# Kernel optimization log

Measured on AMD Instinct MI355X. Metric: run time of the kernel, lower is better.

Reference implementation:

```python
import jax, jax.numpy as jnp
import numpy as np

DIM = 2048        # model hidden size
INTER = 1408      # per-expert intermediate size
E = 16            # n_routed_experts
TOPK = 2          # n_activated_experts
S_INTER = 2816    # shared experts intermediate (n_shared_experts * INTER)
T = 4096          # tokens (batch*seq, module flattens to [-1, dim])
ROUTE_SCALE = 1.0


def setup_inputs() -> dict:
    key = jax.random.key(0)
    ks = jax.random.split(key, 8)
    g = lambda k, shape, scale: (jax.random.normal(k, shape, dtype=jnp.float32) * scale)
    return {
        "x": g(ks[0], (T, DIM), 1.0),
        "gate_w": g(ks[1], (E, DIM), 0.02),
        "w1": g(ks[2], (E, INTER, DIM), 0.02),
        "w2": g(ks[3], (E, DIM, INTER), 0.02),
        "w3": g(ks[4], (E, INTER, DIM), 0.02),
        "sw1": g(ks[5], (S_INTER, DIM), 0.02),
        "sw2": g(ks[6], (DIM, S_INTER), 0.02),
        "sw3": g(ks[7], (S_INTER, DIM), 0.02),
    }


def _moe_forward(x, gate_w, w1, w2, w3, sw1, sw2, sw3):
    t = x.shape[0]
    # ---- gate: softmax scores -> top-k experts per token ----
    scores = jax.nn.softmax(x @ gate_w.T, axis=-1)          # [T, E]
    top_w, top_i = jax.lax.top_k(scores, TOPK)              # [T, K]
    top_w = top_w * ROUTE_SCALE
    # dense combine weights [T, E]: zero for unselected experts
    combine = jnp.zeros((t, E), x.dtype).at[jnp.arange(t)[:, None], top_i].add(top_w)
    # ---- routed experts: gated silu MLP per expert, weighted combine ----
    # loop over the small fixed expert count; tokens with combine==0 contribute 0,
    # matching the original scatter/gather dispatch math exactly.
    y = jnp.zeros_like(x)
    for e in range(E):
        h = jax.nn.silu(x @ w1[e].T) * (x @ w3[e].T)        # [T, INTER]
        y = y + (h @ w2[e].T) * combine[:, e:e + 1]
    # ---- shared experts ----
    z = (jax.nn.silu(x @ sw1.T) * (x @ sw3.T)) @ sw2.T      # [T, DIM]
    return y + z


def reference(x, gate_w, w1, w2, w3, sw1, sw2, sw3):
    return _moe_forward(x, gate_w, w1, w2, w3, sw1, sw2, sw3)
```

## Files before the change

kernel.cpp:

```cpp
#include <hip/hip_runtime.h>
#include <hip/hip_bf16.h>
#include <cstdint>
#include <cstddef>

#define TTOK   4096
#define DIM_   2048
#define INTER_ 1408
#define NEXP   16
#define SINTER_ 2816
#define BM 128
#define BN 128
#define BK 32
#define MAXROWS (TTOK*2 + NEXP*BM)
#define MAXMT   (TTOK*2/BM + NEXP)

typedef unsigned short u16;
typedef __attribute__((ext_vector_type(8))) short short8;
typedef __attribute__((ext_vector_type(4))) float f32x4;

#define AS3P(p) ((__attribute__((address_space(3))) void*)(p))
#define AS1P(p) ((const __attribute__((address_space(1))) void*)(p))

__device__ __forceinline__ void gll16(const void* g, void* l) {
    __builtin_amdgcn_global_load_lds(AS1P(g), AS3P(l), 16, 0, 0);
}

__device__ __forceinline__ u16 f2bf(float f) {
    __hip_bfloat16 h = __float2bfloat16(f);
    union { __hip_bfloat16 h; u16 u; } c; c.h = h; return c.u;
}

__device__ __forceinline__ unsigned pk2(float a, float b) {
    unsigned r;
    asm("v_cvt_pk_bf16_f32 %0, %1, %2" : "=v"(r) : "v"(a), "v"(b));
    return r;
}

__device__ __forceinline__ short8 cvt8(float4 q0, float4 q1) {
    union { int4 i; short8 s; } u;
    u.i = make_int4((int)pk2(q0.x, q0.y), (int)pk2(q0.z, q0.w),
                    (int)pk2(q1.x, q1.y), (int)pk2(q1.z, q1.w));
    return u.s;
}

__device__ __forceinline__ int4 pack8(float4 a, float4 b) {
    int4 r;
    r.x = (int)pk2(a.x, a.y);
    r.y = (int)pk2(a.z, a.w);
    r.z = (int)pk2(b.x, b.y);
    r.w = (int)pk2(b.z, b.w);
    return r;
}


__global__ void init_kernel(int* perm_rt, float* pw_rt, int* perm_sh, int* misc, int* zrow) {
    int i = blockIdx.x * 256 + threadIdx.x;
    if (i < MAXROWS) { perm_rt[i] = -1; pw_rt[i] = 0.f; }
    if (i < TTOK)    perm_sh[i] = i;
    if (i < 32)      misc[i] = 0;
    if (i < 1024)    zrow[i] = 0;
}

__global__ void cvt_kernel(const float* __restrict__ s, u16* __restrict__ d, int n8) {
    int stride = gridDim.x * 256;
    for (int i = blockIdx.x * 256 + threadIdx.x; i < n8; i += stride) {
        const float4* s4 = (const float4*)(s + (size_t)i * 8);
        float4 a = s4[0], b = s4[1];
        *(int4*)(d + (size_t)i * 8) = pack8(a, b);
    }
}

__global__ void gate_kernel(const float* __restrict__ x, const float* __restrict__ gw,
                            int* __restrict__ topi, float* __restrict__ topw,
                            int* __restrict__ misc) {
    int t = blockIdx.x;
    int lane = threadIdx.x;
    const float* xr = x + (size_t)t * DIM_;
    float acc[NEXP];
#pragma unroll
    for (int e = 0; e < NEXP; e++) acc[e] = 0.f;
#pragma unroll
    for (int i = 0; i < 8; i++) {
        int k = i * 256 + lane * 4;
        float4 xv = *(const float4*)(xr + k);
#pragma unroll
        for (int e = 0; e < NEXP; e++) {
            float4 gv = *(const float4*)(gw + (size_t)e * DIM_ + k);
            acc[e] += xv.x * gv.x + xv.y * gv.y + xv.z * gv.z + xv.w * gv.w;
        }
    }
#pragma unroll
    for (int e = 0; e < NEXP; e++) {
        float v = acc[e];
        for (int off = 32; off > 0; off >>= 1) v += __shfl_down(v, off);
        acc[e] = v;
    }
    if (lane == 0) {
        float m = acc[0];
#pragma unroll
        for (int e = 1; e < NEXP; e++) m = fmaxf(m, acc[e]);
        float p[NEXP]; float s = 0.f;
#pragma unroll
        for (int e = 0; e < NEXP; e++) { p[e] = __expf(acc[e] - m); s += p[e]; }
        int i0 = 0; float v0 = p[0];
#pragma unroll
        for (int e = 1; e < NEXP; e++) if (p[e] > v0) { v0 = p[e]; i0 = e; }
        int i1 = -1; float v1 = -1.f;
#pragma unroll
        for (int e = 0; e < NEXP; e++) if (e != i0 && p[e] > v1) { v1 = p[e]; i1 = e; }
        float inv = 1.f / s;
        topi[2 * t] = i0; topi[2 * t + 1] = i1;
        topw[2 * t] = v0 * inv; topw[2 * t + 1] = v1 * inv;
        atomicAdd(&misc[i0], 1);
        atomicAdd(&misc[i1], 1);
    }
}

__global__ void scan_kernel(int* misc) {
    int* counts = misc;
    int* base   = misc + 32;
    int* te     = misc + 48;
    int* tr     = misc + 128;
    int b = 0, tt = 0;
    for (int e = 0; e < NEXP; e++) {
        int c = counts[e];
        int nt = (c + BM - 1) >> 7;
        base[e] = b;
        for (int i = 0; i < nt; i++) { te[tt] = e; tr[tt] = b + i * BM; tt++; }
        b += nt * BM;
    }
    for (int i = tt; i < MAXMT; i++) te[i] = -1;
}

__global__ void scatter_kernel(const int* __restrict__ topi, const float* __restrict__ topw,
                               int* __restrict__ misc, int* __restrict__ perm,
                               float* __restrict__ pw) {
    int t = blockIdx.x * 256 + threadIdx.x;
    if (t >= TTOK) return;
    int* fill = misc + 16;
    int* base = misc + 32;
#pragma unroll
    for (int k = 0; k < 2; k++) {
        int e = topi[2 * t + k];
        int pos = base[e] + atomicAdd(&fill[e], 1);
        perm[pos] = t;
        pw[pos] = topw[2 * t + k];
    }
}


template<bool GROUPED>
__global__ __launch_bounds__(256, 2) void gemm_h13_k(
    const u16* __restrict__ Xb,
    const float* __restrict__ W1b, const float* __restrict__ W3b,
    u16* __restrict__ H,
    const int* __restrict__ perm,
    const int* __restrict__ te, const int* __restrict__ tr,
    const u16* __restrict__ zrow,
    int N, int K, int nt_m, int chunk)
{
    const int q = (blockIdx.x & 7) * chunk + (blockIdx.x >> 3);
    if (q >= nt_m * (N / BN)) return;
    const int jn = q / nt_m, im = q % nt_m;
    int e, slot0;
    if (GROUPED) { e = te[im]; if (e < 0) return; slot0 = tr[im]; }
    else         { e = 0; slot0 = im * BM; }
    const int n0 = jn * BN;
    const float* W1 = W1b + (size_t)e * N * K;
    const float* W3 = W3b + (size_t)e * N * K;

    __shared__ __align__(16) u16   As[BM * BK];
    __shared__ __align__(16) float B1f[BM * BK];
    __shared__ __align__(16) float B3f[BM * BK];

    const int tid = threadIdx.x;
    const int lane = tid & 63, wid = tid >> 6;
    const int wr = wid >> 1, wc = wid & 1;
    const int col = lane & 15, kg = lane >> 4;

    const int aRow = wid * 32 + (lane >> 2);
    const int aCk  = ((lane & 3) ^ ((lane >> 3) & 3)) * 8;
    const int ta0 = perm[slot0 + aRow];
    const int ta1 = perm[slot0 + aRow + 16];
    const u16* ga0 = (ta0 >= 0 ? Xb + (size_t)ta0 * K : zrow) + aCk;
    const u16* ga1 = (ta1 >= 0 ? Xb + (size_t)ta1 * K : zrow) + aCk;
    u16* la0 = As + (wid * 32) * BK;
    u16* la1 = As + (wid * 32 + 16) * BK;

    const int bRowL = lane >> 3;
    const int bCk   = ((lane & 7) ^ bRowL) * 4;
    const float* g1 = W1 + (size_t)(n0 + wid * 32 + bRowL) * K + bCk;
    const float* g3 = W3 + (size_t)(n0 + wid * 32 + bRowL) * K + bCk;
    float* lb1 = B1f + (wid * 32) * BK;
    float* lb3 = B3f + (wid * 32) * BK;

    const int aswz = (col >> 1) & 3;
    const int bswz = col & 7;

    f32x4 acc1[4][4] = {};
    f32x4 acc3[4][4] = {};

    for (int k0 = 0; k0 < K; k0 += BK) {
        gll16(ga0 + k0, la0);
        gll16(ga1 + k0, la1);
#pragma unroll
        for (int j = 0; j < 4; j++) {
            gll16(g1 + (size_t)j * 8 * K + k0, lb1 + j * 8 * BK);
            gll16(g3 + (size_t)j * 8 * K + k0, lb3 + j * 8 * BK);
        }
        __syncthreads();

        short8 a[4];
#pragma unroll
        for (int mi = 0; mi < 4; mi++)
            a[mi] = *(const short8*)(As + (wr * 64 + mi * 16 + col) * BK + ((kg ^ aswz) * 8));
#pragma unroll
        for (int ni = 0; ni < 4; ni++) {
            const int rowB = wc * 64 + ni * 16 + col;
            const float* rb1 = B1f + rowB * BK;
            const float* rb3 = B3f + rowB * BK;
            const int c0 = ((kg * 2) ^ bswz) * 4;
            const int c1 = ((kg * 2 + 1) ^ bswz) * 4;
            short8 v1 = cvt8(*(const float4*)(rb1 + c0), *(const float4*)(rb1 + c1));
            short8 v3 = cvt8(*(const float4*)(rb3 + c0), *(const float4*)(rb3 + c1));
#pragma unroll
            for (int mi = 0; mi < 4; mi++) {
                acc1[mi][ni] = __builtin_amdgcn_mfma_f32_16x16x32_bf16(a[mi], v1, acc1[mi][ni], 0, 0, 0);
                acc3[mi][ni] = __builtin_amdgcn_mfma_f32_16x16x32_bf16(a[mi], v3, acc3[mi][ni], 0, 0, 0);
            }
        }
        __syncthreads();
    }

#pragma unroll
    for (int mi = 0; mi < 4; mi++) {
#pragma unroll
        for (int j = 0; j < 4; j++) {
            int row = slot0 + wr * 64 + mi * 16 + kg * 4 + j;
#pragma unroll
            for (int ni = 0; ni < 4; ni++) {
                float v1 = acc1[mi][ni][j];
                float v3 = acc3[mi][ni][j];
                float hv = v1 / (1.f + __expf(-v1)) * v3;
                int c = n0 + wc * 64 + ni * 16 + col;
                H[(size_t)row * N + c] = f2bf(hv);
            }
        }
    }
}

template<bool ATOMIC>
__global__ __launch_bounds__(256, 2) void gemm_out_k(
    const u16* __restrict__ Hm,
    const float* __restrict__ W2b,
    float* __restrict__ Out,
    const int* __restrict__ perm, const float* __restrict__ pw,
    const int* __restrict__ te, const int* __restrict__ tr,
    int K, int nt_m, int chunk)
{
    const int q = (blockIdx.x & 7) * chunk + (blockIdx.x >> 3);
    if (q >= nt_m * (DIM_ / BN)) return;
    const int jn = q / nt_m, im = q % nt_m;
    int e, slot0;
    if (ATOMIC) { e = te[im]; if (e < 0) return; slot0 = tr[im]; }
    else        { e = 0; slot0 = im * BM; }
    const int n0 = jn * BN;
    const float* W2 = W2b + (size_t)e * DIM_ * K;

    __shared__ __align__(16) u16   As[BM * BK];
    __shared__ __align__(16) float Bf[BM * BK];

    const int tid = threadIdx.x;
    const int lane = tid & 63, wid = tid >> 6;
    const int wr = wid >> 1, wc = wid & 1;
    const int col = lane & 15, kg = lane >> 4;

    const int aRow = wid * 32 + (lane >> 2);
    const int aCk  = ((lane & 3) ^ ((lane >> 3) & 3)) * 8;
    const u16* ga0 = Hm + (size_t)(slot0 + aRow) * K + aCk;
    const u16* ga1 = Hm + (size_t)(slot0 + aRow + 16) * K + aCk;
    u16* la0 = As + (wid * 32) * BK;
    u16* la1 = As + (wid * 32 + 16) * BK;

    const int bRowL = lane >> 3;
    const int bCk   = ((lane & 7) ^ bRowL) * 4;
    const float* g2 = W2 + (size_t)(n0 + wid * 32 + bRowL) * K + bCk;
    float* lb = Bf + (wid * 32) * BK;

    const int aswz = (col >> 1) & 3;
    const int bswz = col & 7;

    f32x4 acc[4][4] = {};

    for (int k0 = 0; k0 < K; k0 += BK) {
        gll16(ga0 + k0, la0);
        gll16(ga1 + k0, la1);
#pragma unroll
        for (int j = 0; j < 4; j++)
            gll16(g2 + (size_t)j * 8 * K + k0, lb + j * 8 * BK);
        __syncthreads();

        short8 a[4];
#pragma unroll
        for (int mi = 0; mi < 4; mi++)
            a[mi] = *(const short8*)(As + (wr * 64 + mi * 16 + col) * BK + ((kg ^ aswz) * 8));
#pragma unroll
        for (int ni = 0; ni < 4; ni++) {
            const int rowB = wc * 64 + ni * 16 + col;
            const float* rb = Bf + rowB * BK;
            const int c0 = ((kg * 2) ^ bswz) * 4;
            const int c1 = ((kg * 2 + 1) ^ bswz) * 4;
            short8 bv = cvt8(*(const float4*)(rb + c0), *(const float4*)(rb + c1));
#pragma unroll
            for (int mi = 0; mi < 4; mi++)
                acc[mi][ni] = __builtin_amdgcn_mfma_f32_16x16x32_bf16(a[mi], bv, acc[mi][ni], 0, 0, 0);
        }
        __syncthreads();
    }

#pragma unroll
    for (int mi = 0; mi < 4; mi++) {
#pragma unroll
        for (int j = 0; j < 4; j++) {
            int rloc = wr * 64 + mi * 16 + kg * 4 + j;
            int slot = slot0 + rloc;
            if (ATOMIC) {
                int token = perm[slot];
                if (token < 0) continue;
                float w = pw[slot];
#pragma unroll
                for (int ni = 0; ni < 4; ni++) {
                    int c = n0 + wc * 64 + ni * 16 + col;
                    atomicAdd(&Out[(size_t)token * DIM_ + c], acc[mi][ni][j] * w);
                }
            } else {
#pragma unroll
                for (int ni = 0; ni < 4; ni++) {
                    int c = n0 + wc * 64 + ni * 16 + col;
                    Out[(size_t)slot * DIM_ + c] = acc[mi][ni][j];
                }
            }
        }
    }
}


extern "C" void kernel_launch(void* const* d_in, const int* in_sizes, int n_in,
                              void* d_out, int out_size, void* d_ws, size_t ws_size,
                              hipStream_t stream) {
    (void)in_sizes; (void)n_in; (void)out_size; (void)ws_size;
    const float* x   = (const float*)d_in[0];
    const float* gw  = (const float*)d_in[1];
    const float* w1  = (const float*)d_in[2];
    const float* w2  = (const float*)d_in[3];
    const float* w3  = (const float*)d_in[4];
    const float* sw1 = (const float*)d_in[5];
    const float* sw2 = (const float*)d_in[6];
    const float* sw3 = (const float*)d_in[7];
    float* out = (float*)d_out;

    char* ws = (char*)d_ws;
    size_t off = 0;
    auto take = [&](size_t bytes) -> void* {
        void* p = ws + off;
        off += (bytes + 255) & ~(size_t)255;
        return p;
    };
    u16*   xb      = (u16*)take((size_t)TTOK * DIM_ * 2);
    u16*   hbuf    = (u16*)take((size_t)MAXROWS * INTER_ * 2);
    int*   perm_rt = (int*)take((size_t)MAXROWS * 4);
    float* pw_rt   = (float*)take((size_t)MAXROWS * 4);
    int*   perm_sh = (int*)take((size_t)TTOK * 4);
    int*   topi    = (int*)take((size_t)TTOK * 2 * 4);
    float* topw    = (float*)take((size_t)TTOK * 2 * 4);
    int*   misc    = (int*)take(1024);
    int*   zrow    = (int*)take(4096);

    init_kernel<<<MAXROWS / 256, 256, 0, stream>>>(perm_rt, pw_rt, perm_sh, misc, zrow);
    cvt_kernel<<<512, 256, 0, stream>>>(x, xb, TTOK * DIM_ / 8);
    gate_kernel<<<TTOK, 64, 0, stream>>>(x, gw, topi, topw, misc);
    scan_kernel<<<1, 1, 0, stream>>>(misc);
    scatter_kernel<<<TTOK / 256, 256, 0, stream>>>(topi, topw, misc, perm_rt, pw_rt);

    auto grid8 = [](int total) { return ((total + 7) / 8) * 8; };
    auto chunk8 = [](int total) { return (total + 7) / 8; };

    {
        int total = (TTOK / BM) * (SINTER_ / BN);
        gemm_h13_k<false><<<grid8(total), 256, 0, stream>>>(
            xb, sw1, sw3, hbuf, perm_sh, nullptr, nullptr, (const u16*)zrow,
            SINTER_, DIM_, TTOK / BM, chunk8(total));
    }
    {
        int total = (TTOK / BM) * (DIM_ / BN);
        gemm_out_k<false><<<grid8(total), 256, 0, stream>>>(
            hbuf, sw2, out, nullptr, nullptr, nullptr, nullptr,
            SINTER_, TTOK / BM, chunk8(total));
    }
    {
        int total = MAXMT * (INTER_ / BN);
        gemm_h13_k<true><<<grid8(total), 256, 0, stream>>>(
            xb, w1, w3, hbuf, perm_rt, misc + 48, misc + 128, (const u16*)zrow,
            INTER_, DIM_, MAXMT, chunk8(total));
    }
    {
        int total = MAXMT * (DIM_ / BN);
        gemm_out_k<true><<<grid8(total), 256, 0, stream>>>(
            hbuf, w2, out, perm_rt, pw_rt, misc + 48, misc + 128,
            INTER_, MAXMT, chunk8(total));
    }
}
```

Before: 879.0 us.

## Double-buffer LDS tiles in gate/up and down GEMMs to overlap loads with MFMA

Both GEMM kernels now keep two LDS buffers per operand. The next K-tile is issued via global_load_lds before computing on the current tile, and an explicit vmcnt(0) wait plus barrier replaces the two syncthreads per iteration. The aim is to hide global memory latency behind the MFMA work. The cost is double the LDS footprint: the gate/up kernel goes from about 40KB to 80KB, which may reduce occupancy.

Result: no change. 876.5 us (-0.3%).

```diff
diff --git a/kernel.cpp b/kernel.cpp
--- a/kernel.cpp
+++ b/kernel.cpp
@@ -51,6 +51,12 @@
     r.w = (int)pk2(b.z, b.w);
     return r;
 }
+
+#define WAIT_VM0_BARRIER() do { \
+    asm volatile("s_waitcnt vmcnt(0)" ::: "memory"); \
+    __builtin_amdgcn_s_barrier(); \
+    asm volatile("" ::: "memory"); \
+} while (0)
 
 
 __global__ void init_kernel(int* perm_rt, float* pw_rt, int* perm_sh, int* misc, int* zrow) {
@@ -169,9 +175,9 @@
     const float* W1 = W1b + (size_t)e * N * K;
     const float* W3 = W3b + (size_t)e * N * K;
 
-    __shared__ __align__(16) u16   As[BM * BK];
-    __shared__ __align__(16) float B1f[BM * BK];
-    __shared__ __align__(16) float B3f[BM * BK];
+    __shared__ __align__(16) u16   As[2][BM * BK];
+    __shared__ __align__(16) float B1f[2][BM * BK];
+    __shared__ __align__(16) float B3f[2][BM * BK];
 
     const int tid = threadIdx.x;
     const int lane = tid & 63, wid = tid >> 6;
@@ -184,15 +190,14 @@
     const int ta1 = perm[slot0 + aRow + 16];
     const u16* ga0 = (ta0 >= 0 ? Xb + (size_t)ta0 * K : zrow) + aCk;
     const u16* ga1 = (ta1 >= 0 ? Xb + (size_t)ta1 * K : zrow) + aCk;
-    u16* la0 = As + (wid * 32) * BK;
-    u16* la1 = As + (wid * 32 + 16) * BK;
+    const int laOff0 = (wid * 32) * BK;
+    const int laOff1 = (wid * 32 + 16) * BK;
 
     const int bRowL = lane >> 3;
     const int bCk   = ((lane & 7) ^ bRowL) * 4;
     const float* g1 = W1 + (size_t)(n0 + wid * 32 + bRowL) * K + bCk;
     const float* g3 = W3 + (size_t)(n0 + wid * 32 + bRowL) * K + bCk;
-    float* lb1 = B1f + (wid * 32) * BK;
-    float* lb3 = B3f + (wid * 32) * BK;
+    const int lbOff = (wid * 32) * BK;
 
     const int aswz = (col >> 1) & 3;
     const int bswz = col & 7;
@@ -200,25 +205,44 @@
     f32x4 acc1[4][4] = {};
     f32x4 acc3[4][4] = {};
 
+    {
+        gll16(ga0, &As[0][laOff0]);
+        gll16(ga1, &As[0][laOff1]);
+#pragma unroll
+        for (int j = 0; j < 4; j++) {
+            gll16(g1 + (size_t)j * 8 * K, &B1f[0][lbOff + j * 8 * BK]);
+            gll16(g3 + (size_t)j * 8 * K, &B3f[0][lbOff + j * 8 * BK]);
+        }
+    }
+    WAIT_VM0_BARRIER();
+
+    int cur = 0;
     for (int k0 = 0; k0 < K; k0 += BK) {
-        gll16(ga0 + k0, la0);
-        gll16(ga1 + k0, la1);
-#pragma unroll
-        for (int j = 0; j < 4; j++) {
-            gll16(g1 + (size_t)j * 8 * K + k0, lb1 + j * 8 * BK);
-            gll16(g3 + (size_t)j * 8 * K + k0, lb3 + j * 8 * BK);
-        }
-        __syncthreads();
+        const int kn = k0 + BK;
+        if (kn < K) {
+            const int nb = cur ^ 1;
+            gll16(ga0 + kn, &As[nb][laOff0]);
+            gll16(ga1 + kn, &As[nb][laOff1]);
+#pragma unroll
+            for (int j = 0; j < 4; j++) {
+                gll16(g1 + (size_t)j * 8 * K + kn, &B1f[nb][lbOff + j * 8 * BK]);
+                gll16(g3 + (size_t)j * 8 * K + kn, &B3f[nb][lbOff + j * 8 * BK]);
+            }
+        }
+
+        const u16*   Ac  = As[cur];
+        const float* B1c = B1f[cur];
+        const float* B3c = B3f[cur];
 
         short8 a[4];
 #pragma unroll
         for (int mi = 0; mi < 4; mi++)
-            a[mi] = *(const short8*)(As + (wr * 64 + mi * 16 + col) * BK + ((kg ^ aswz) * 8));
+            a[mi] = *(const short8*)(Ac + (wr * 64 + mi * 16 + col) * BK + ((kg ^ aswz) * 8));
 #pragma unroll
         for (int ni = 0; ni < 4; ni++) {
             const int rowB = wc * 64 + ni * 16 + col;
-            const float* rb1 = B1f + rowB * BK;
-            const float* rb3 = B3f + rowB * BK;
+            const float* rb1 = B1c + rowB * BK;
+            const float* rb3 = B3c + rowB * BK;
             const int c0 = ((kg * 2) ^ bswz) * 4;
             const int c1 = ((kg * 2 + 1) ^ bswz) * 4;
             short8 v1 = cvt8(*(const float4*)(rb1 + c0), *(const float4*)(rb1 + c1));
@@ -229,7 +253,9 @@
                 acc3[mi][ni] = __builtin_amdgcn_mfma_f32_16x16x32_bf16(a[mi], v3, acc3[mi][ni], 0, 0, 0);
             }
         }
-        __syncthreads();
+
+        WAIT_VM0_BARRIER();
+        cur ^= 1;
     }
 
 #pragma unroll
@@ -267,8 +293,8 @@
     const int n0 = jn * BN;
     const float* W2 = W2b + (size_t)e * DIM_ * K;
 
-    __shared__ __align__(16) u16   As[BM * BK];
-    __shared__ __align__(16) float Bf[BM * BK];
+    __shared__ __align__(16) u16   As[2][BM * BK];
+    __shared__ __align__(16) float Bf[2][BM * BK];
 
     const int tid = threadIdx.x;
     const int lane = tid & 63, wid = tid >> 6;
@@ -279,35 +305,51 @@
     const int aCk  = ((lane & 3) ^ ((lane >> 3) & 3)) * 8;
     const u16* ga0 = Hm + (size_t)(slot0 + aRow) * K + aCk;
     const u16* ga1 = Hm + (size_t)(slot0 + aRow + 16) * K + aCk;
-    u16* la0 = As + (wid * 32) * BK;
-    u16* la1 = As + (wid * 32 + 16) * BK;
+    const int laOff0 = (wid * 32) * BK;
+    const int laOff1 = (wid * 32 + 16) * BK;
 
     const int bRowL = lane >> 3;
     const int bCk   = ((lane & 7) ^ bRowL) * 4;
     const float* g2 = W2 + (size_t)(n0 + wid * 32 + bRowL) * K + bCk;
-    float* lb = Bf + (wid * 32) * BK;
+    const int lbOff = (wid * 32) * BK;
 
     const int aswz = (col >> 1) & 3;
     const int bswz = col & 7;
 
     f32x4 acc[4][4] = {};
 
+    {
+        gll16(ga0, &As[0][laOff0]);
+        gll16(ga1, &As[0][laOff1]);
+#pragma unroll
+        for (int j = 0; j < 4; j++)
+            gll16(g2 + (size_t)j * 8 * K, &Bf[0][lbOff + j * 8 * BK]);
+    }
+    WAIT_VM0_BARRIER();
+
+    int cur = 0;
     for (int k0 = 0; k0 < K; k0 += BK) {
-        gll16(ga0 + k0, la0);
-        gll16(ga1 + k0, la1);
-#pragma unroll
-        for (int j = 0; j < 4; j++)
-            gll16(g2 + (size_t)j * 8 * K + k0, lb + j * 8 * BK);
-        __syncthreads();
+        const int kn = k0 + BK;
+        if (kn < K) {
+            const int nb = cur ^ 1;
+            gll16(ga0 + kn, &As[nb][laOff0]);
+            gll16(ga1 + kn, &As[nb][laOff1]);
+#pragma unroll
+            for (int j = 0; j < 4; j++)
+                gll16(g2 + (size_t)j * 8 * K + kn, &Bf[nb][lbOff + j * 8 * BK]);
+        }
+
+        const u16*   Ac = As[cur];
+        const float* Bc = Bf[cur];
 
         short8 a[4];
 #pragma unroll
         for (int mi = 0; mi < 4; mi++)
-            a[mi] = *(const short8*)(As + (wr * 64 + mi * 16 + col) * BK + ((kg ^ aswz) * 8));
+            a[mi] = *(const short8*)(Ac + (wr * 64 + mi * 16 + col) * BK + ((kg ^ aswz) * 8));
 #pragma unroll
         for (int ni = 0; ni < 4; ni++) {
             const int rowB = wc * 64 + ni * 16 + col;
-            const float* rb = Bf + rowB * BK;
+            const float* rb = Bc + rowB * BK;
             const int c0 = ((kg * 2) ^ bswz) * 4;
             const int c1 = ((kg * 2 + 1) ^ bswz) * 4;
             short8 bv = cvt8(*(const float4*)(rb + c0), *(const float4*)(rb + c1));
@@ -315,7 +357,9 @@
             for (int mi = 0; mi < 4; mi++)
                 acc[mi][ni] = __builtin_amdgcn_mfma_f32_16x16x32_bf16(a[mi], bv, acc[mi][ni], 0, 0, 0);
         }
-        __syncthreads();
+
+        WAIT_VM0_BARRIER();
+        cur ^= 1;
     }
 
 #pragma unroll
```

## Pre-convert all weight matrices to bf16 before the GEMMs

Applied to the files above, without the earlier changes.

Adds per-call conversion passes that turn the fp32 expert and shared weights into bf16 workspace buffers. The GEMM kernels now load bf16 B tiles straight into LDS with the same swizzle as the A tiles, so the per-tile fp32-to-bf16 conversion in the inner loop goes away and weight bytes per tile load are halved. The cost is a full extra read and write over roughly 600MB of fp32 weights on every call, plus a larger workspace. The cvt launch grid for x is also enlarged.

After: 864.0 us. About the same (-1.7%).

```diff
diff --git a/kernel.cpp b/kernel.cpp
--- a/kernel.cpp
+++ b/kernel.cpp
@@ -34,13 +34,6 @@
     unsigned r;
     asm("v_cvt_pk_bf16_f32 %0, %1, %2" : "=v"(r) : "v"(a), "v"(b));
     return r;
-}
-
-__device__ __forceinline__ short8 cvt8(float4 q0, float4 q1) {
-    union { int4 i; short8 s; } u;
-    u.i = make_int4((int)pk2(q0.x, q0.y), (int)pk2(q0.z, q0.w),
-                    (int)pk2(q1.x, q1.y), (int)pk2(q1.z, q1.w));
-    return u.s;
 }
 
 __device__ __forceinline__ int4 pack8(float4 a, float4 b) {
@@ -152,7 +145,7 @@
 template<bool GROUPED>
 __global__ __launch_bounds__(256, 2) void gemm_h13_k(
     const u16* __restrict__ Xb,
-    const float* __restrict__ W1b, const float* __restrict__ W3b,
+    const u16* __restrict__ W1b, const u16* __restrict__ W3b,
     u16* __restrict__ H,
     const int* __restrict__ perm,
     const int* __restrict__ te, const int* __restrict__ tr,
@@ -166,36 +159,37 @@
     if (GROUPED) { e = te[im]; if (e < 0) return; slot0 = tr[im]; }
     else         { e = 0; slot0 = im * BM; }
     const int n0 = jn * BN;
-    const float* W1 = W1b + (size_t)e * N * K;
-    const float* W3 = W3b + (size_t)e * N * K;
-
-    __shared__ __align__(16) u16   As[BM * BK];
-    __shared__ __align__(16) float B1f[BM * BK];
-    __shared__ __align__(16) float B3f[BM * BK];
+    const u16* W1 = W1b + (size_t)e * N * K;
+    const u16* W3 = W3b + (size_t)e * N * K;
+
+    __shared__ __align__(16) u16 As[BM * BK];
+    __shared__ __align__(16) u16 B1s[BM * BK];
+    __shared__ __align__(16) u16 B3s[BM * BK];
 
     const int tid = threadIdx.x;
     const int lane = tid & 63, wid = tid >> 6;
     const int wr = wid >> 1, wc = wid & 1;
     const int col = lane & 15, kg = lane >> 4;
 
-    const int aRow = wid * 32 + (lane >> 2);
-    const int aCk  = ((lane & 3) ^ ((lane >> 3) & 3)) * 8;
-    const int ta0 = perm[slot0 + aRow];
-    const int ta1 = perm[slot0 + aRow + 16];
-    const u16* ga0 = (ta0 >= 0 ? Xb + (size_t)ta0 * K : zrow) + aCk;
-    const u16* ga1 = (ta1 >= 0 ? Xb + (size_t)ta1 * K : zrow) + aCk;
-    u16* la0 = As + (wid * 32) * BK;
-    u16* la1 = As + (wid * 32 + 16) * BK;
-
-    const int bRowL = lane >> 3;
-    const int bCk   = ((lane & 7) ^ bRowL) * 4;
-    const float* g1 = W1 + (size_t)(n0 + wid * 32 + bRowL) * K + bCk;
-    const float* g3 = W3 + (size_t)(n0 + wid * 32 + bRowL) * K + bCk;
-    float* lb1 = B1f + (wid * 32) * BK;
-    float* lb3 = B3f + (wid * 32) * BK;
-
-    const int aswz = (col >> 1) & 3;
-    const int bswz = col & 7;
+    const int lr = lane >> 2;
+    const int kb = ((lane & 3) ^ ((lane >> 3) & 3)) * 8;
+    const int ar0 = wid * 32 + lr, ar1 = ar0 + 16;
+    const int ta0 = perm[slot0 + ar0];
+    const int ta1 = perm[slot0 + ar1];
+    const u16* ga0 = (ta0 >= 0 ? Xb + (size_t)ta0 * K : zrow) + kb;
+    const u16* ga1 = (ta1 >= 0 ? Xb + (size_t)ta1 * K : zrow) + kb;
+    const u16* gb1a = W1 + (size_t)(n0 + ar0) * K + kb;
+    const u16* gb1b = W1 + (size_t)(n0 + ar1) * K + kb;
+    const u16* gb3a = W3 + (size_t)(n0 + ar0) * K + kb;
+    const u16* gb3b = W3 + (size_t)(n0 + ar1) * K + kb;
+    u16* la0 = As  + (wid * 32) * BK;
+    u16* la1 = As  + (wid * 32 + 16) * BK;
+    u16* lb1a = B1s + (wid * 32) * BK;
+    u16* lb1b = B1s + (wid * 32 + 16) * BK;
+    u16* lb3a = B3s + (wid * 32) * BK;
+    u16* lb3b = B3s + (wid * 32 + 16) * BK;
+
+    const int sw = (col >> 1) & 3;
 
     f32x4 acc1[4][4] = {};
     f32x4 acc3[4][4] = {};
@@ -203,26 +197,21 @@
     for (int k0 = 0; k0 < K; k0 += BK) {
         gll16(ga0 + k0, la0);
         gll16(ga1 + k0, la1);
-#pragma unroll
-        for (int j = 0; j < 4; j++) {
-            gll16(g1 + (size_t)j * 8 * K + k0, lb1 + j * 8 * BK);
-            gll16(g3 + (size_t)j * 8 * K + k0, lb3 + j * 8 * BK);
-        }
+        gll16(gb1a + k0, lb1a);
+        gll16(gb1b + k0, lb1b);
+        gll16(gb3a + k0, lb3a);
+        gll16(gb3b + k0, lb3b);
         __syncthreads();
 
         short8 a[4];
 #pragma unroll
         for (int mi = 0; mi < 4; mi++)
-            a[mi] = *(const short8*)(As + (wr * 64 + mi * 16 + col) * BK + ((kg ^ aswz) * 8));
+            a[mi] = *(const short8*)(As + (wr * 64 + mi * 16 + col) * BK + ((kg ^ sw) * 8));
 #pragma unroll
         for (int ni = 0; ni < 4; ni++) {
-            const int rowB = wc * 64 + ni * 16 + col;
-            const float* rb1 = B1f + rowB * BK;
-            const float* rb3 = B3f + rowB * BK;
-            const int c0 = ((kg * 2) ^ bswz) * 4;
-            const int c1 = ((kg * 2 + 1) ^ bswz) * 4;
-            short8 v1 = cvt8(*(const float4*)(rb1 + c0), *(const float4*)(rb1 + c1));
-            short8 v3 = cvt8(*(const float4*)(rb3 + c0), *(const float4*)(rb3 + c1));
+            const int rowB = (wc * 64 + ni * 16 + col) * BK + ((kg ^ sw) * 8);
+            short8 v1 = *(const short8*)(B1s + rowB);
+            short8 v3 = *(const short8*)(B3s + rowB);
 #pragma unroll
             for (int mi = 0; mi < 4; mi++) {
                 acc1[mi][ni] = __builtin_amdgcn_mfma_f32_16x16x32_bf16(a[mi], v1, acc1[mi][ni], 0, 0, 0);
@@ -252,7 +241,7 @@
 template<bool ATOMIC>
 __global__ __launch_bounds__(256, 2) void gemm_out_k(
     const u16* __restrict__ Hm,
-    const float* __restrict__ W2b,
+    const u16* __restrict__ W2b,
     float* __restrict__ Out,
     const int* __restrict__ perm, const float* __restrict__ pw,
     const int* __restrict__ te, const int* __restrict__ tr,
@@ -265,52 +254,46 @@
     if (ATOMIC) { e = te[im]; if (e < 0) return; slot0 = tr[im]; }
     else        { e = 0; slot0 = im * BM; }
     const int n0 = jn * BN;
-    const float* W2 = W2b + (size_t)e * DIM_ * K;
-
-    __shared__ __align__(16) u16   As[BM * BK];
-    __shared__ __align__(16) float Bf[BM * BK];
+    const u16* W2 = W2b + (size_t)e * DIM_ * K;
+
+    __shared__ __align__(16) u16 As[BM * BK];
+    __shared__ __align__(16) u16 Bs[BM * BK];
 
     const int tid = threadIdx.x;
     const int lane = tid & 63, wid = tid >> 6;
     const int wr = wid >> 1, wc = wid & 1;
     const int col = lane & 15, kg = lane >> 4;
 
-    const int aRow = wid * 32 + (lane >> 2);
-    const int aCk  = ((lane & 3) ^ ((lane >> 3) & 3)) * 8;
-    const u16* ga0 = Hm + (size_t)(slot0 + aRow) * K + aCk;
-    const u16* ga1 = Hm + (size_t)(slot0 + aRow + 16) * K + aCk;
+    const int lr = lane >> 2;
+    const int kb = ((lane & 3) ^ ((lane >> 3) & 3)) * 8;
+    const int ar0 = wid * 32 + lr, ar1 = ar0 + 16;
+    const u16* ga0 = Hm + (size_t)(slot0 + ar0) * K + kb;
+    const u16* ga1 = Hm + (size_t)(slot0 + ar1) * K + kb;
+    const u16* gb0 = W2 + (size_t)(n0 + ar0) * K + kb;
+    const u16* gb1 = W2 + (size_t)(n0 + ar1) * K + kb;
     u16* la0 = As + (wid * 32) * BK;
     u16* la1 = As + (wid * 32 + 16) * BK;
-
-    const int bRowL = lane >> 3;
-    const int bCk   = ((lane & 7) ^ bRowL) * 4;
-    const float* g2 = W2 + (size_t)(n0 + wid * 32 + bRowL) * K + bCk;
-    float* lb = Bf + (wid * 32) * BK;
-
-    const int aswz = (col >> 1) & 3;
-    const int bswz = col & 7;
+    u16* lb0 = Bs + (wid * 32) * BK;
+    u16* lb1 = Bs + (wid * 32 + 16) * BK;
+
+    const int sw = (col >> 1) & 3;
 
     f32x4 acc[4][4] = {};
 
     for (int k0 = 0; k0 < K; k0 += BK) {
         gll16(ga0 + k0, la0);
         gll16(ga1 + k0, la1);
-#pragma unroll
-        for (int j = 0; j < 4; j++)
-            gll16(g2 + (size_t)j * 8 * K + k0, lb + j * 8 * BK);
+        gll16(gb0 + k0, lb0);
+        gll16(gb1 + k0, lb1);
         __syncthreads();
 
         short8 a[4];
 #pragma unroll
         for (int mi = 0; mi < 4; mi++)
-            a[mi] = *(const short8*)(As + (wr * 64 + mi * 16 + col) * BK + ((kg ^ aswz) * 8));
+            a[mi] = *(const short8*)(As + (wr * 64 + mi * 16 + col) * BK + ((kg ^ sw) * 8));
 #pragma unroll
         for (int ni = 0; ni < 4; ni++) {
-            const int rowB = wc * 64 + ni * 16 + col;
-            const float* rb = Bf + rowB * BK;
-            const int c0 = ((kg * 2) ^ bswz) * 4;
-            const int c1 = ((kg * 2 + 1) ^ bswz) * 4;
-            short8 bv = cvt8(*(const float4*)(rb + c0), *(const float4*)(rb + c1));
+            short8 bv = *(const short8*)(Bs + (wc * 64 + ni * 16 + col) * BK + ((kg ^ sw) * 8));
 #pragma unroll
             for (int mi = 0; mi < 4; mi++)
                 acc[mi][ni] = __builtin_amdgcn_mfma_f32_16x16x32_bf16(a[mi], bv, acc[mi][ni], 0, 0, 0);
@@ -375,38 +358,53 @@
     float* topw    = (float*)take((size_t)TTOK * 2 * 4);
     int*   misc    = (int*)take(1024);
     int*   zrow    = (int*)take(4096);
+    const size_t nW  = (size_t)NEXP * INTER_ * DIM_;
+    const size_t nSW = (size_t)SINTER_ * DIM_;
+    u16* w1b  = (u16*)take(nW * 2);
+    u16* w2b  = (u16*)take(nW * 2);
+    u16* w3b  = (u16*)take(nW * 2);
+    u16* sw1b = (u16*)take(nSW * 2);
+    u16* sw2b = (u16*)take(nSW * 2);
+    u16* sw3b = (u16*)take(nSW * 2);
 
     init_kernel<<<MAXROWS / 256, 256, 0, stream>>>(perm_rt, pw_rt, perm_sh, misc, zrow);
-    cvt_kernel<<<512, 256, 0, stream>>>(x, xb, TTOK * DIM_ / 8);
+    cvt_kernel<<<2048, 256, 0, stream>>>(x, xb, TTOK * DIM_ / 8);
     gate_kernel<<<TTOK, 64, 0, stream>>>(x, gw, topi, topw, misc);
     scan_kernel<<<1, 1, 0, stream>>>(misc);
     scatter_kernel<<<TTOK / 256, 256, 0, stream>>>(topi, topw, misc, perm_rt, pw_rt);
 
+    cvt_kernel<<<4096, 256, 0, stream>>>(w1,  w1b,  (int)(nW / 8));
+    cvt_kernel<<<4096, 256, 0, stream>>>(w2,  w2b,  (int)(nW / 8));
+    cvt_kernel<<<4096, 256, 0, stream>>>(w3,  w3b,  (int)(nW / 8));
+    cvt_kernel<<<4096, 256, 0, stream>>>(sw1, sw1b, (int)(nSW / 8));
+    cvt_kernel<<<4096, 256, 0, stream>>>(sw2, sw2b, (int)(nSW / 8));
+    cvt_kernel<<<4096, 256, 0, stream>>>(sw3, sw3b, (int)(nSW / 8));
+
     auto grid8 = [](int total) { return ((total + 7) / 8) * 8; };
     auto chunk8 = [](int total) { return (total + 7) / 8; };
 
     {
         int total = (TTOK / BM) * (SINTER_ / BN);
         gemm_h13_k<false><<<grid8(total), 256, 0, stream>>>(
-            xb, sw1, sw3, hbuf, perm_sh, nullptr, nullptr, (const u16*)zrow,
+            xb, sw1b, sw3b, hbuf, perm_sh, nullptr, nullptr, (const u16*)zrow,
             SINTER_, DIM_, TTOK / BM, chunk8(total));
     }
     {
         int total = (TTOK / BM) * (DIM_ / BN);
         gemm_out_k<false><<<grid8(total), 256, 0, stream>>>(
-            hbuf, sw2, out, nullptr, nullptr, nullptr, nullptr,
+            hbuf, sw2b, out, nullptr, nullptr, nullptr, nullptr,
             SINTER_, TTOK / BM, chunk8(total));
     }
     {
         int total = MAXMT * (INTER_ / BN);
         gemm_h13_k<true><<<grid8(total), 256, 0, stream>>>(
-            xb, w1, w3, hbuf, perm_rt, misc + 48, misc + 128, (const u16*)zrow,
+            xb, w1b, w3b, hbuf, perm_rt, misc + 48, misc + 128, (const u16*)zrow,
             INTER_, DIM_, MAXMT, chunk8(total));
     }
     {
         int total = MAXMT * (DIM_ / BN);
         gemm_out_k<true><<<grid8(total), 256, 0, stream>>>(
-            hbuf, w2, out, perm_rt, pw_rt, misc + 48, misc + 128,
+            hbuf, w2b, out, perm_rt, pw_rt, misc + 48, misc + 128,
             INTER_, MAXMT, chunk8(total));
     }
 }
```
